# Kernel tuning notes

Measured on AMD Instinct MI355X. Metric: run time of the kernel, lower is better.

Reference implementation:

```python
import jax, jax.numpy as jnp
import numpy as np


def setup_inputs() -> dict:
    key = jax.random.key(0)
    k1, k2 = jax.random.split(key)
    n_task, shot, feat, n_class = 32, 2048, 1024, 512
    inputs = jax.random.normal(k1, (n_task, shot, feat), dtype=jnp.float32)
    weights = jax.random.normal(k2, (n_task, n_class, feat), dtype=jnp.float32)
    return {"inputs": inputs, "weights": weights, "temp": 15}


def reference(inputs, weights, temp):
    # logits[t,s,c] = temp * (x.w - 0.5*||w||^2 - 0.5*||x||^2)
    dots = jnp.einsum('tsf,tcf->tsc', inputs, weights)        # [T,S,C]
    w_sq = 0.5 * jnp.sum(weights * weights, axis=2)           # [T,C]
    x_sq = 0.5 * jnp.sum(inputs * inputs, axis=2)             # [T,S]
    logits = temp * (dots - w_sq[:, None, :] - x_sq[:, :, None])
    return jnp.argmax(logits, axis=2)                         # [T,S] int
```

## Files before the change

### kernel.cpp

```cpp
#include <hip/hip_runtime.h>
#include <cstdint>
#include <cstddef>

#define T_TASKS 32
#define S_SHOT  2048
#define F_FEAT  1024
#define C_CLS   512
#define MARGIN  0.1f
#define NBLK    (T_TASKS * (S_SHOT / 64))

typedef _Float16 f16;
typedef _Float16 f16x4 __attribute__((ext_vector_type(4)));
typedef _Float16 f16x8 __attribute__((ext_vector_type(8)));
typedef float    f32x4 __attribute__((ext_vector_type(4)));

__device__ __forceinline__ void gl_lds16(const void* g, void* l) {
  auto gp = (const __attribute__((address_space(1))) uint32_t*)(g);
  auto lp = (__attribute__((address_space(3))) uint32_t*)(l);
  __builtin_amdgcn_global_load_lds(gp, lp, 16, 0, 0);
}

__device__ __forceinline__ void upd3(float v, int i,
                                     float& v1, int& i1,
                                     float& v2, int& i2,
                                     float& v3, int& i3) {
  if (v > v1 || (v == v1 && i < i1)) { v3=v2; i3=i2; v2=v1; i2=i1; v1=v; i1=i; }
  else if (v > v2 || (v == v2 && i < i2)) { v3=v2; i3=i2; v2=v; i2=i; }
  else if (v > v3 || (v == v3 && i < i3)) { v3=v; i3=i; }
}

__global__ __launch_bounds__(256) void prep_w(const float* __restrict__ W,
                                              f16* __restrict__ Wh,
                                              float* __restrict__ wsq) {
  int rid = blockIdx.x * 4 + (threadIdx.x >> 6);
  int ln  = threadIdx.x & 63;
  int c   = rid & (C_CLS - 1);
  int t   = rid >> 9;
  const float* wr = W + (size_t)rid * F_FEAT;
  double s = 0.0;
#pragma unroll
  for (int j = 0; j < 4; ++j) {
    int f = (j * 64 + ln) * 4;
    float4 v = *(const float4*)(wr + f);
    s += (double)v.x * v.x + (double)v.y * v.y +
         (double)v.z * v.z + (double)v.w * v.w;
    f16x4 h;
    h.x = (f16)v.x; h.y = (f16)v.y; h.z = (f16)v.z; h.w = (f16)v.w;
    int kt = f >> 5;
    int q  = (f >> 3) & 3;
    int jj = f & 7;
    int u  = c * 4 + ((q + (c >> 1)) & 3);
    size_t off = ((size_t)(t * 32 + kt) << 14) + (size_t)u * 8 + jj;
    *(f16x4*)(Wh + off) = h;
  }
#pragma unroll
  for (int off = 32; off > 0; off >>= 1) s += __shfl_xor(s, off);
  if (ln == 0) wsq[rid] = (float)(0.5 * s);
}

struct MainSh {
  f16 W0[16384];
  f16 W1[16384];
  f16 Xh[64 * 40];
  f16 Xl[64 * 40];
};
struct EpiSh {
  float  swsq[C_CLS];
  float  cv[64][2][3];
  int    ci[64][2][3];
  double rs[48];
  int    amb_cnt;
  int    amb_list[64];
};
union ShU { MainSh m; EpiSh e; };

__device__ __forceinline__ void issue_w8(const f16* Wht, f16* dst, int ktn,
                                         int wv, int ln) {
  const f16* g = Wht + ((size_t)ktn << 14) + wv * 4096 + ln * 8;
  f16* l = dst + wv * 4096;
#pragma unroll
  for (int i = 0; i < 8; ++i) gl_lds16(g + i * 512, l + i * 512);
}

__device__ __forceinline__ void cvt_write_x(float4 a, float4 b,
                                            f16* xwh, f16* xwl) {
  f16x4 h, l;
  h.x = (f16)a.x; l.x = (f16)(a.x - (float)h.x);
  h.y = (f16)a.y; l.y = (f16)(a.y - (float)h.y);
  h.z = (f16)a.z; l.z = (f16)(a.z - (float)h.z);
  h.w = (f16)a.w; l.w = (f16)(a.w - (float)h.w);
  *(f16x4*)(xwh) = h;
  *(f16x4*)(xwl) = l;
  h.x = (f16)b.x; l.x = (f16)(b.x - (float)h.x);
  h.y = (f16)b.y; l.y = (f16)(b.y - (float)h.y);
  h.z = (f16)b.z; l.z = (f16)(b.z - (float)h.z);
  h.w = (f16)b.w; l.w = (f16)(b.w - (float)h.w);
  *(f16x4*)(xwh + 32 * 40) = h;
  *(f16x4*)(xwl + 32 * 40) = l;
}

__global__ __launch_bounds__(256, 2) void gemm_argmax(
    const float* __restrict__ X, const float* __restrict__ W,
    const f16* __restrict__ Wh, const float* __restrict__ wsq,
    int* __restrict__ out) {
  __shared__ __align__(16) ShU sh;

  const int tid = threadIdx.x;
  const int wv  = tid >> 6, ln = tid & 63;
  const int rg  = wv >> 1, cg = wv & 1;
  const int m   = ln & 15, q = ln >> 4;

  int bx = blockIdx.x;
  bx = (bx & 7) * (NBLK / 8) + (bx >> 3);
  const int t    = bx >> 5, rb = bx & 31;
  const int row0 = rb * 64;

  const float* Xblk = X + ((size_t)t * S_SHOT + row0) * F_FEAT;
  const f16*   Wht  = Wh + ((size_t)(t * 32) << 14);

  const int sr = tid >> 3, sq = tid & 7;
  const float* xg0 = Xblk + (size_t)sr * F_FEAT + sq * 4;
  const float* xg1 = xg0 + (size_t)32 * F_FEAT;
  f16* xwh = sh.m.Xh + sr * 40 + sq * 4;
  f16* xwl = sh.m.Xl + sr * 40 + sq * 4;

  const f16* aph = sh.m.Xh + (rg * 32 + m) * 40 + q * 8;
  const f16* apl = sh.m.Xl + (rg * 32 + m) * 40 + q * 8;
  const int c0 = cg * 256 + m;
  const int u0 = c0 * 4 + ((q + (c0 >> 1)) & 3);

  const f32x4 zero4 = {0.f, 0.f, 0.f, 0.f};
  f32x4 acc[2][16];
#pragma unroll
  for (int a = 0; a < 2; ++a)
#pragma unroll
    for (int b = 0; b < 16; ++b) acc[a][b] = zero4;

  f16* Wr = sh.m.W0;
  f16* Ws = sh.m.W1;

  {
    float4 a = *(const float4*)(xg0);
    float4 b = *(const float4*)(xg1);
    issue_w8(Wht, Wr, 0, wv, ln);
    cvt_write_x(a, b, xwh, xwl);
    asm volatile("s_waitcnt vmcnt(0)" ::: "memory");
    asm volatile("s_waitcnt lgkmcnt(0)" ::: "memory");
    __builtin_amdgcn_s_barrier();
  }

#pragma unroll 1
  for (int kt = 0; kt < 32; ++kt) {
    const bool more = (kt < 31);
    float4 a, b;
    if (more) {
      a = *(const float4*)(xg0 + (kt + 1) * 32);
      b = *(const float4*)(xg1 + (kt + 1) * 32);
      issue_w8(Wht, Ws, kt + 1, wv, ln);
    }
    f16x8 ah0 = *(const f16x8*)(aph);
    f16x8 ah1 = *(const f16x8*)(aph + 16 * 40);
    f16x8 al0 = *(const f16x8*)(apl);
    f16x8 al1 = *(const f16x8*)(apl + 16 * 40);
    asm volatile("s_waitcnt lgkmcnt(0)" ::: "memory");
    __builtin_amdgcn_s_barrier();

    __builtin_amdgcn_s_setprio(1);
    const f16* bp = Wr + u0 * 8;
#pragma unroll
    for (int ct = 0; ct < 16; ++ct) {
      f16x8 bh = *(const f16x8*)(bp + ct * 512);
      acc[0][ct] = __builtin_amdgcn_mfma_f32_16x16x32_f16(ah0, bh, acc[0][ct], 0, 0, 0);
      acc[0][ct] = __builtin_amdgcn_mfma_f32_16x16x32_f16(al0, bh, acc[0][ct], 0, 0, 0);
      acc[1][ct] = __builtin_amdgcn_mfma_f32_16x16x32_f16(ah1, bh, acc[1][ct], 0, 0, 0);
      acc[1][ct] = __builtin_amdgcn_mfma_f32_16x16x32_f16(al1, bh, acc[1][ct], 0, 0, 0);
    }
    __builtin_amdgcn_s_setprio(0);

    if (more) cvt_write_x(a, b, xwh, xwl);
    asm volatile("s_waitcnt vmcnt(0)" ::: "memory");
    asm volatile("s_waitcnt lgkmcnt(0)" ::: "memory");
    __builtin_amdgcn_s_barrier();
    f16* tmp = Wr; Wr = Ws; Ws = tmp;
  }
  __syncthreads();

  sh.e.swsq[tid]       = wsq[t * C_CLS + tid];
  sh.e.swsq[tid + 256] = wsq[t * C_CLS + tid + 256];
  if (tid == 0) sh.e.amb_cnt = 0;
  __syncthreads();

#pragma unroll
  for (int rt = 0; rt < 2; ++rt) {
#pragma unroll
    for (int rr = 0; rr < 4; ++rr) {
      float v1 = -3.4e38f, v2 = -3.4e38f, v3 = -3.4e38f;
      int   i1 = 0x7fffffff, i2 = 0x7fffffff, i3 = 0x7fffffff;
#pragma unroll
      for (int ct = 0; ct < 16; ++ct) {
        int cidx = c0 + ct * 16;
        float sc = acc[rt][ct][rr] - sh.e.swsq[cidx];
        upd3(sc, cidx, v1, i1, v2, i2, v3, i3);
      }
      for (int off = 1; off < 16; off <<= 1) {
        float w1 = __shfl_xor(v1, off); int j1 = __shfl_xor(i1, off);
        float w2 = __shfl_xor(v2, off); int j2 = __shfl_xor(i2, off);
        float w3 = __shfl_xor(v3, off); int j3 = __shfl_xor(i3, off);
        upd3(w1, j1, v1, i1, v2, i2, v3, i3);
        upd3(w2, j2, v1, i1, v2, i2, v3, i3);
        upd3(w3, j3, v1, i1, v2, i2, v3, i3);
      }
      if (m == 0) {
        int row = rg * 32 + rt * 16 + q * 4 + rr;
        sh.e.cv[row][cg][0] = v1; sh.e.ci[row][cg][0] = i1;
        sh.e.cv[row][cg][1] = v2; sh.e.ci[row][cg][1] = i2;
        sh.e.cv[row][cg][2] = v3; sh.e.ci[row][cg][2] = i3;
      }
    }
  }
  __syncthreads();

  if (tid < 64) {
    float a1 = sh.e.cv[tid][0][0]; int aj = sh.e.ci[tid][0][0];
    float b1 = sh.e.cv[tid][1][0]; int bj = sh.e.ci[tid][1][0];
    float win, runner; int widx;
    if (a1 > b1 || (a1 == b1 && aj < bj)) {
      win = a1; widx = aj; runner = fmaxf(b1, sh.e.cv[tid][0][1]);
    } else {
      win = b1; widx = bj; runner = fmaxf(a1, sh.e.cv[tid][1][1]);
    }
    if (win - runner >= MARGIN) {
      out[t * S_SHOT + row0 + tid] = widx;
    } else {
      int p = atomicAdd(&sh.e.amb_cnt, 1);
      sh.e.amb_list[p] = tid;
    }
  }
  __syncthreads();

  int nA = sh.e.amb_cnt;
  for (int base = 0; base < nA; base += 8) {
    int nr = nA - base; if (nr > 8) nr = 8;
    int np = nr * 6;
    for (int p = wv; p < np; p += 4) {
      int rrow = p / 6;
      int cand = p - rrow * 6;
      int rl   = sh.e.amb_list[base + rrow];
      int g    = (cand >= 3) ? 1 : 0;
      int k    = cand - g * 3;
      int cidx = sh.e.ci[rl][g][k];
      const float* xr = X + ((size_t)t * S_SHOT + row0 + rl) * F_FEAT;
      const float* wr = W + ((size_t)t * C_CLS + cidx) * F_FEAT;
      double sd = 0.0, sw = 0.0;
#pragma unroll
      for (int j = 0; j < 16; ++j) {
        float xv  = xr[ln + 64 * j];
        float wv2 = wr[ln + 64 * j];
        sd += (double)xv * (double)wv2;
        sw += (double)wv2 * (double)wv2;
      }
#pragma unroll
      for (int off = 32; off > 0; off >>= 1) {
        sd += __shfl_xor(sd, off);
        sw += __shfl_xor(sw, off);
      }
      if (ln == 0) sh.e.rs[p] = sd - 0.5 * sw;
    }
    __syncthreads();
    if (tid < nr) {
      int rl = sh.e.amb_list[base + tid];
      double best = -1.0e300; int bidx = 0x7fffffff;
#pragma unroll
      for (int cand = 0; cand < 6; ++cand) {
        int g = cand / 3, k = cand % 3;
        int cidx = sh.e.ci[rl][g][k];
        double sc = sh.e.rs[tid * 6 + cand];
        if (sc > best || (sc == best && cidx < bidx)) { best = sc; bidx = cidx; }
      }
      out[t * S_SHOT + row0 + rl] = bidx;
    }
    __syncthreads();
  }
}

extern "C" void kernel_launch(void* const* d_in, const int* in_sizes, int n_in,
                              void* d_out, int out_size, void* d_ws, size_t ws_size,
                              hipStream_t stream) {
  (void)in_sizes; (void)n_in; (void)out_size;
  const float* X = (const float*)d_in[0];
  const float* W = (const float*)d_in[1];
  const size_t wh_bytes = (size_t)T_TASKS * C_CLS * F_FEAT * sizeof(f16);
  const size_t need = wh_bytes + (size_t)T_TASKS * C_CLS * sizeof(float);
  if (ws_size < need) return;
  f16*   Wh  = (f16*)d_ws;
  float* wsq = (float*)((char*)d_ws + wh_bytes);
  int*   out = (int*)d_out;
  prep_w<<<T_TASKS * C_CLS / 4, 256, 0, stream>>>(W, Wh, wsq);
  gemm_argmax<<<NBLK, 256, 0, stream>>>(X, W, Wh, wsq, out);
}
```

Before: 793.5 us.

## Load X fragments straight into registers instead of staging through LDS

Each lane now loads its own fp32 slice of X from global memory and splits it into f16 hi/lo MFMA operands in registers. This removes the X staging buffers in LDS and their writes and reads. The k-loop is unrolled by two with fixed W double buffers, and the separate waitcnt/barrier pairs are replaced by a single __syncthreads per step. In exchange, the two column-group waves each fetch the same X rows, which doubles global/L2 traffic for X. Prefetch depth for X now depends on register double-buffering.

```diff
diff --git a/kernel.cpp b/kernel.cpp
--- a/kernel.cpp
+++ b/kernel.cpp
@@ -61,8 +61,6 @@
 struct MainSh {
   f16 W0[16384];
   f16 W1[16384];
-  f16 Xh[64 * 40];
-  f16 Xl[64 * 40];
 };
 struct EpiSh {
   float  swsq[C_CLS];
@@ -82,21 +80,15 @@
   for (int i = 0; i < 8; ++i) gl_lds16(g + i * 512, l + i * 512);
 }
 
-__device__ __forceinline__ void cvt_write_x(float4 a, float4 b,
-                                            f16* xwh, f16* xwl) {
-  f16x4 h, l;
-  h.x = (f16)a.x; l.x = (f16)(a.x - (float)h.x);
-  h.y = (f16)a.y; l.y = (f16)(a.y - (float)h.y);
-  h.z = (f16)a.z; l.z = (f16)(a.z - (float)h.z);
-  h.w = (f16)a.w; l.w = (f16)(a.w - (float)h.w);
-  *(f16x4*)(xwh) = h;
-  *(f16x4*)(xwl) = l;
-  h.x = (f16)b.x; l.x = (f16)(b.x - (float)h.x);
-  h.y = (f16)b.y; l.y = (f16)(b.y - (float)h.y);
-  h.z = (f16)b.z; l.z = (f16)(b.z - (float)h.z);
-  h.w = (f16)b.w; l.w = (f16)(b.w - (float)h.w);
-  *(f16x4*)(xwh + 32 * 40) = h;
-  *(f16x4*)(xwl + 32 * 40) = l;
+__device__ __forceinline__ void cvt8(float4 u, float4 v, f16x8& h, f16x8& l) {
+  h[0] = (f16)u.x; l[0] = (f16)(u.x - (float)h[0]);
+  h[1] = (f16)u.y; l[1] = (f16)(u.y - (float)h[1]);
+  h[2] = (f16)u.z; l[2] = (f16)(u.z - (float)h[2]);
+  h[3] = (f16)u.w; l[3] = (f16)(u.w - (float)h[3]);
+  h[4] = (f16)v.x; l[4] = (f16)(v.x - (float)h[4]);
+  h[5] = (f16)v.y; l[5] = (f16)(v.y - (float)h[5]);
+  h[6] = (f16)v.z; l[6] = (f16)(v.z - (float)h[6]);
+  h[7] = (f16)v.w; l[7] = (f16)(v.w - (float)h[7]);
 }
 
 __global__ __launch_bounds__(256, 2) void gemm_argmax(
@@ -115,17 +107,11 @@
   const int t    = bx >> 5, rb = bx & 31;
   const int row0 = rb * 64;
 
-  const float* Xblk = X + ((size_t)t * S_SHOT + row0) * F_FEAT;
-  const f16*   Wht  = Wh + ((size_t)(t * 32) << 14);
-
-  const int sr = tid >> 3, sq = tid & 7;
-  const float* xg0 = Xblk + (size_t)sr * F_FEAT + sq * 4;
-  const float* xg1 = xg0 + (size_t)32 * F_FEAT;
-  f16* xwh = sh.m.Xh + sr * 40 + sq * 4;
-  f16* xwl = sh.m.Xl + sr * 40 + sq * 4;
-
-  const f16* aph = sh.m.Xh + (rg * 32 + m) * 40 + q * 8;
-  const f16* apl = sh.m.Xl + (rg * 32 + m) * 40 + q * 8;
+  const f16* Wht = Wh + ((size_t)(t * 32) << 14);
+
+  const float* xgA = X + ((size_t)(t * S_SHOT) + row0 + rg * 32 + m) * F_FEAT + q * 8;
+  const float* xgB = xgA + (size_t)16 * F_FEAT;
+
   const int c0 = cg * 256 + m;
   const int u0 = c0 * 4 + ((q + (c0 >> 1)) & 3);
 
@@ -136,53 +122,48 @@
 #pragma unroll
     for (int b = 0; b < 16; ++b) acc[a][b] = zero4;
 
-  f16* Wr = sh.m.W0;
-  f16* Ws = sh.m.W1;
-
-  {
-    float4 a = *(const float4*)(xg0);
-    float4 b = *(const float4*)(xg1);
-    issue_w8(Wht, Wr, 0, wv, ln);
-    cvt_write_x(a, b, xwh, xwl);
-    asm volatile("s_waitcnt vmcnt(0)" ::: "memory");
-    asm volatile("s_waitcnt lgkmcnt(0)" ::: "memory");
-    __builtin_amdgcn_s_barrier();
+  issue_w8(Wht, sh.m.W0, 0, wv, ln);
+  float4 xa0 = *(const float4*)(xgA);
+  float4 xa1 = *(const float4*)(xgA + 4);
+  float4 xb0 = *(const float4*)(xgB);
+  float4 xb1 = *(const float4*)(xgB + 4);
+
+#define KSTEP(KT, WRD, WST, PRED)                                            \
+  {                                                                          \
+    __syncthreads();                                                         \
+    const bool pr_ = (PRED);                                                 \
+    if (pr_) issue_w8(Wht, (WST), (KT) + 1, wv, ln);                         \
+    float4 na0, na1, nb0, nb1;                                               \
+    if (pr_) {                                                               \
+      const float* pA_ = xgA + ((KT) + 1) * 32;                              \
+      const float* pB_ = xgB + ((KT) + 1) * 32;                              \
+      na0 = *(const float4*)(pA_); na1 = *(const float4*)(pA_ + 4);          \
+      nb0 = *(const float4*)(pB_); nb1 = *(const float4*)(pB_ + 4);          \
+    }                                                                        \
+    f16x8 ah0, al0, ah1, al1;                                                \
+    cvt8(xa0, xa1, ah0, al0);                                                \
+    cvt8(xb0, xb1, ah1, al1);                                                \
+    __builtin_amdgcn_s_setprio(1);                                           \
+    const f16* bp_ = (WRD) + u0 * 8;                                         \
+    _Pragma("unroll")                                                        \
+    for (int ct = 0; ct < 16; ++ct) {                                        \
+      f16x8 bh = *(const f16x8*)(bp_ + ct * 512);                            \
+      acc[0][ct] = __builtin_amdgcn_mfma_f32_16x16x32_f16(ah0, bh, acc[0][ct], 0, 0, 0); \
+      acc[0][ct] = __builtin_amdgcn_mfma_f32_16x16x32_f16(al0, bh, acc[0][ct], 0, 0, 0); \
+      acc[1][ct] = __builtin_amdgcn_mfma_f32_16x16x32_f16(ah1, bh, acc[1][ct], 0, 0, 0); \
+      acc[1][ct] = __builtin_amdgcn_mfma_f32_16x16x32_f16(al1, bh, acc[1][ct], 0, 0, 0); \
+    }                                                                        \
+    __builtin_amdgcn_s_setprio(0);                                           \
+    if (pr_) { xa0 = na0; xa1 = na1; xb0 = nb0; xb1 = nb1; }                 \
   }
 
 #pragma unroll 1
-  for (int kt = 0; kt < 32; ++kt) {
-    const bool more = (kt < 31);
-    float4 a, b;
-    if (more) {
-      a = *(const float4*)(xg0 + (kt + 1) * 32);
-      b = *(const float4*)(xg1 + (kt + 1) * 32);
-      issue_w8(Wht, Ws, kt + 1, wv, ln);
-    }
-    f16x8 ah0 = *(const f16x8*)(aph);
-    f16x8 ah1 = *(const f16x8*)(aph + 16 * 40);
-    f16x8 al0 = *(const f16x8*)(apl);
-    f16x8 al1 = *(const f16x8*)(apl + 16 * 40);
-    asm volatile("s_waitcnt lgkmcnt(0)" ::: "memory");
-    __builtin_amdgcn_s_barrier();
-
-    __builtin_amdgcn_s_setprio(1);
-    const f16* bp = Wr + u0 * 8;
-#pragma unroll
-    for (int ct = 0; ct < 16; ++ct) {
-      f16x8 bh = *(const f16x8*)(bp + ct * 512);
-      acc[0][ct] = __builtin_amdgcn_mfma_f32_16x16x32_f16(ah0, bh, acc[0][ct], 0, 0, 0);
-      acc[0][ct] = __builtin_amdgcn_mfma_f32_16x16x32_f16(al0, bh, acc[0][ct], 0, 0, 0);
-      acc[1][ct] = __builtin_amdgcn_mfma_f32_16x16x32_f16(ah1, bh, acc[1][ct], 0, 0, 0);
-      acc[1][ct] = __builtin_amdgcn_mfma_f32_16x16x32_f16(al1, bh, acc[1][ct], 0, 0, 0);
-    }
-    __builtin_amdgcn_s_setprio(0);
-
-    if (more) cvt_write_x(a, b, xwh, xwl);
-    asm volatile("s_waitcnt vmcnt(0)" ::: "memory");
-    asm volatile("s_waitcnt lgkmcnt(0)" ::: "memory");
-    __builtin_amdgcn_s_barrier();
-    f16* tmp = Wr; Wr = Ws; Ws = tmp;
-  }
+  for (int kp = 0; kp < 16; ++kp) {
+    KSTEP(2 * kp,     sh.m.W0, sh.m.W1, true);
+    KSTEP(2 * kp + 1, sh.m.W1, sh.m.W0, kp < 15);
+  }
+#undef KSTEP
+
   __syncthreads();
 
   sh.e.swsq[tid]       = wsq[t * C_CLS + tid];
```

Measured after the change: 824.3 us. 1.04x slower.
